# Kernel tuning notes

Measured on AMD Instinct MI355X. Metric: run time of the kernel, lower is better.

Reference implementation:

```python
import jax, jax.numpy as jnp
import numpy as np

N_NODES = 100000
N_EDGES = 1600000
IN_DIM = 128
HID = 128
NUM_LAYERS = 10
NUM_CLASSES = 2
NUM_GRAPHS = 64


def setup_inputs() -> dict:
    key = jax.random.key(0)
    ks = jax.random.split(key, 16)
    x = jax.random.normal(ks[0], (N_NODES, IN_DIM), dtype=jnp.float32)
    # edges with no self loops (GIN_Conv calls remove_self_loops)
    src = jax.random.randint(ks[1], (N_EDGES,), 0, N_NODES)
    off = jax.random.randint(ks[2], (N_EDGES,), 1, N_NODES)
    dst = (src + off) % N_NODES
    edge_index = jnp.stack([src, dst]).astype(jnp.int64)
    batch = jnp.sort(jax.random.randint(ks[3], (N_NODES,), 0, NUM_GRAPHS)).astype(jnp.int64)
    s = 1.0 / np.sqrt(HID)
    eps = jnp.zeros((NUM_LAYERS,), dtype=jnp.float32)
    W1 = jax.random.normal(ks[4], (NUM_LAYERS, IN_DIM, HID), dtype=jnp.float32) * s
    b1 = jnp.zeros((NUM_LAYERS, HID), dtype=jnp.float32)
    W2 = jax.random.normal(ks[5], (NUM_LAYERS, HID, HID), dtype=jnp.float32) * s
    b2 = jnp.zeros((NUM_LAYERS, HID), dtype=jnp.float32)
    Wc1 = jax.random.normal(ks[6], (HID, HID), dtype=jnp.float32) * s
    bc1 = jnp.zeros((HID,), dtype=jnp.float32)
    Wc2 = jax.random.normal(ks[7], (HID, NUM_CLASSES), dtype=jnp.float32) * s
    bc2 = jnp.zeros((NUM_CLASSES,), dtype=jnp.float32)
    return {"x": x, "edge_index": edge_index, "batch": batch, "eps": eps,
            "W1": W1, "b1": b1, "W2": W2, "b2": b2,
            "Wc1": Wc1, "bc1": bc1, "Wc2": Wc2, "bc2": bc2}


def _gin_block(x, src, dst, eps_i, W1_i, b1_i, W2_i, b2_i, mlp_residual):
    # gather-scatter add aggregation: aggr[v] = sum_{(u->v)} x[u]
    aggr = jax.ops.segment_sum(x[src], dst, num_segments=N_NODES)
    h = (1.0 + eps_i) * x + aggr
    out = jnp.dot(jax.nn.relu(jnp.dot(h, W1_i) + b1_i), W2_i) + b2_i
    if mlp_residual:  # MLP internal residual (layers i > 0)
        out = out + h
    out = jax.nn.relu(out)  # ResidualGNNBlock: Identity norm, relu, Identity dropout
    out = out + x  # block residual (dims match: in_dim == hidden)
    return out


def reference(x, edge_index, batch, eps, W1, b1, W2, b2, Wc1, bc1, Wc2, bc2):
    src, dst = edge_index[0], edge_index[1]
    for i in range(NUM_LAYERS):
        x = _gin_block(x, src, dst, eps[i], W1[i], b1[i], W2[i], b2[i], mlp_residual=(i > 0))
    # global_mean_pool
    sums = jax.ops.segment_sum(x, batch, num_segments=NUM_GRAPHS)
    cnts = jax.ops.segment_sum(jnp.ones((x.shape[0], 1), x.dtype), batch, num_segments=NUM_GRAPHS)
    pooled = sums / jnp.maximum(cnts, 1.0)
    # classifier MLP (dropout inactive in eval)
    logits = jnp.dot(jax.nn.relu(jnp.dot(pooled, Wc1) + bc1), Wc2) + bc2
    return logits
```

## Files before the change

### kernel.cpp

```cpp
#include <hip/hip_runtime.h>

#define N_NODES 100000
#define N_EDGES 1600000
#define HID 128
#define NUM_LAYERS 10
#define NUM_GRAPHS 64
#define SCAN_BLOCKS ((N_NODES + 255) / 256)


__global__ __launch_bounds__(256) void count_deg_kernel(const int* __restrict__ dst,
                                                        int* __restrict__ deg, int E) {
  int e = blockIdx.x * 256 + threadIdx.x;
  if (e < E) atomicAdd(&deg[dst[e]], 1);
}

__global__ __launch_bounds__(256) void block_sum_kernel(const int* __restrict__ deg,
                                                        int* __restrict__ psum, int n) {
  __shared__ int sd[256];
  int i = blockIdx.x * 256 + threadIdx.x;
  sd[threadIdx.x] = (i < n) ? deg[i] : 0;
  __syncthreads();
  for (int off = 128; off > 0; off >>= 1) {
    if (threadIdx.x < off) sd[threadIdx.x] += sd[threadIdx.x + off];
    __syncthreads();
  }
  if (threadIdx.x == 0) psum[blockIdx.x] = sd[0];
}

__global__ __launch_bounds__(512) void scan_partials_kernel(const int* __restrict__ psum,
                                                            int* __restrict__ poff, int nb) {
  __shared__ int sd[512];
  int i = threadIdx.x;
  int v = (i < nb) ? psum[i] : 0;
  sd[i] = v;
  __syncthreads();
  for (int off = 1; off < 512; off <<= 1) {
    int t = (i >= off) ? sd[i - off] : 0;
    __syncthreads();
    sd[i] += t;
    __syncthreads();
  }
  if (i < nb) poff[i] = sd[i] - v;
}

__global__ __launch_bounds__(256) void write_rs_kernel(const int* __restrict__ deg,
                                                       const int* __restrict__ poff,
                                                       int* __restrict__ rs, int n) {
  __shared__ int sd[256];
  int i = blockIdx.x * 256 + threadIdx.x;
  int v = (i < n) ? deg[i] : 0;
  sd[threadIdx.x] = v;
  __syncthreads();
  for (int off = 1; off < 256; off <<= 1) {
    int t = (threadIdx.x >= off) ? sd[threadIdx.x - off] : 0;
    __syncthreads();
    sd[threadIdx.x] += t;
    __syncthreads();
  }
  if (i < n) rs[i + 1] = poff[blockIdx.x] + sd[threadIdx.x];
  if (i == 0) rs[0] = 0;
}

__global__ __launch_bounds__(256) void copy_int_kernel(const int* __restrict__ a,
                                                       int* __restrict__ b, int n) {
  int i = blockIdx.x * 256 + threadIdx.x;
  if (i < n) b[i] = a[i];
}

__global__ __launch_bounds__(256) void fill_csr_kernel(const int* __restrict__ src,
                                                       const int* __restrict__ dst,
                                                       int* __restrict__ cur,
                                                       int* __restrict__ csr, int E) {
  int e = blockIdx.x * 256 + threadIdx.x;
  if (e < E) {
    int p = atomicAdd(&cur[dst[e]], 1);
    csr[p] = src[e];
  }
}


__global__ __launch_bounds__(256, 4) void layer_kernel(const float* __restrict__ xin,
                                                       float* __restrict__ xout,
                                                       const int* __restrict__ rs,
                                                       const int* __restrict__ csr,
                                                       const float* __restrict__ eps, int layer,
                                                       const float* __restrict__ W1,
                                                       const float* __restrict__ b1,
                                                       const float* __restrict__ W2,
                                                       const float* __restrict__ b2,
                                                       int n, int addH) {
  __shared__ float lh[64 * 128];
  const int tid = threadIdx.x;
  const int row0 = blockIdx.x * 64;
  const float4* x4 = (const float4*)xin;
  float4* lh4 = (float4*)lh;
  const float s = 1.0f + eps[layer];

  const int w = tid >> 5;
  const int lane = tid & 31;
#pragma unroll
  for (int it = 0; it < 8; ++it) {
    int li = it * 8 + w;
    int node = row0 + li;
    float ax = 0.f, ay = 0.f, az = 0.f, aw = 0.f;
    if (node < n) {
      float4 v = x4[node * 32 + lane];
      ax = v.x * s; ay = v.y * s; az = v.z * s; aw = v.w * s;
      int e = rs[node], e1 = rs[node + 1];
      for (; e + 1 < e1; e += 2) {
        int u0 = csr[e], u1 = csr[e + 1];
        float4 t0 = x4[u0 * 32 + lane];
        float4 t1 = x4[u1 * 32 + lane];
        ax += t0.x; ay += t0.y; az += t0.z; aw += t0.w;
        ax += t1.x; ay += t1.y; az += t1.z; aw += t1.w;
      }
      if (e < e1) {
        int u = csr[e];
        float4 t = x4[u * 32 + lane];
        ax += t.x; ay += t.y; az += t.z; aw += t.w;
      }
    }
    float4 r; r.x = ax; r.y = ay; r.z = az; r.w = aw;
    lh4[li * 32 + lane] = r;
  }
  __syncthreads();

  const int cg = tid & 31;
  const int rg = tid >> 5;
  float acc[8][4];
#pragma unroll
  for (int r = 0; r < 8; ++r) { acc[r][0] = acc[r][1] = acc[r][2] = acc[r][3] = 0.f; }

  for (int k4 = 0; k4 < 32; ++k4) {
    float4 w0 = *(const float4*)(W1 + (k4 * 4 + 0) * 128 + cg * 4);
    float4 w1 = *(const float4*)(W1 + (k4 * 4 + 1) * 128 + cg * 4);
    float4 w2 = *(const float4*)(W1 + (k4 * 4 + 2) * 128 + cg * 4);
    float4 w3 = *(const float4*)(W1 + (k4 * 4 + 3) * 128 + cg * 4);
#pragma unroll
    for (int r = 0; r < 8; ++r) {
      float4 a = *(const float4*)(lh + (rg * 8 + r) * 128 + k4 * 4);
      acc[r][0] += a.x * w0.x + a.y * w1.x + a.z * w2.x + a.w * w3.x;
      acc[r][1] += a.x * w0.y + a.y * w1.y + a.z * w2.y + a.w * w3.y;
      acc[r][2] += a.x * w0.z + a.y * w1.z + a.z * w2.z + a.w * w3.z;
      acc[r][3] += a.x * w0.w + a.y * w1.w + a.z * w2.w + a.w * w3.w;
    }
  }

  float4 hreg[8];
#pragma unroll
  for (int r = 0; r < 8; ++r) hreg[r] = *(const float4*)(lh + (rg * 8 + r) * 128 + cg * 4);
  __syncthreads();

  {
    float4 bb = *(const float4*)(b1 + cg * 4);
#pragma unroll
    for (int r = 0; r < 8; ++r) {
      float4 o;
      o.x = fmaxf(acc[r][0] + bb.x, 0.f);
      o.y = fmaxf(acc[r][1] + bb.y, 0.f);
      o.z = fmaxf(acc[r][2] + bb.z, 0.f);
      o.w = fmaxf(acc[r][3] + bb.w, 0.f);
      *(float4*)(lh + (rg * 8 + r) * 128 + cg * 4) = o;
      acc[r][0] = acc[r][1] = acc[r][2] = acc[r][3] = 0.f;
    }
  }
  __syncthreads();

  for (int k4 = 0; k4 < 32; ++k4) {
    float4 w0 = *(const float4*)(W2 + (k4 * 4 + 0) * 128 + cg * 4);
    float4 w1 = *(const float4*)(W2 + (k4 * 4 + 1) * 128 + cg * 4);
    float4 w2 = *(const float4*)(W2 + (k4 * 4 + 2) * 128 + cg * 4);
    float4 w3 = *(const float4*)(W2 + (k4 * 4 + 3) * 128 + cg * 4);
#pragma unroll
    for (int r = 0; r < 8; ++r) {
      float4 a = *(const float4*)(lh + (rg * 8 + r) * 128 + k4 * 4);
      acc[r][0] += a.x * w0.x + a.y * w1.x + a.z * w2.x + a.w * w3.x;
      acc[r][1] += a.x * w0.y + a.y * w1.y + a.z * w2.y + a.w * w3.y;
      acc[r][2] += a.x * w0.z + a.y * w1.z + a.z * w2.z + a.w * w3.z;
      acc[r][3] += a.x * w0.w + a.y * w1.w + a.z * w2.w + a.w * w3.w;
    }
  }

  float4 b2v = *(const float4*)(b2 + cg * 4);
  float4* xo4 = (float4*)xout;
#pragma unroll
  for (int r = 0; r < 8; ++r) {
    int row = row0 + rg * 8 + r;
    if (row < n) {
      float ox = acc[r][0] + b2v.x;
      float oy = acc[r][1] + b2v.y;
      float oz = acc[r][2] + b2v.z;
      float ow = acc[r][3] + b2v.w;
      if (addH) {
        ox += hreg[r].x; oy += hreg[r].y; oz += hreg[r].z; ow += hreg[r].w;
      }
      ox = fmaxf(ox, 0.f); oy = fmaxf(oy, 0.f); oz = fmaxf(oz, 0.f); ow = fmaxf(ow, 0.f);
      float4 xv = x4[row * 32 + cg];
      float4 o;
      o.x = ox + xv.x; o.y = oy + xv.y; o.z = oz + xv.z; o.w = ow + xv.w;
      xo4[row * 32 + cg] = o;
    }
  }
}


__global__ __launch_bounds__(128) void pool_kernel(const float* __restrict__ x,
                                                   const int* __restrict__ batch,
                                                   float* __restrict__ pool,
                                                   int* __restrict__ gcnt, int n) {
  const int CH = 512;
  int c = threadIdx.x;
  int n0 = blockIdx.x * CH;
  if (n0 >= n) return;
  int n1 = n0 + CH; if (n1 > n) n1 = n;
  float acc = 0.f;
  int g = batch[n0];
  int cl = 0;
  for (int i = n0; i < n1; ++i) {
    int gi = batch[i];
    if (gi != g) {
      atomicAdd(&pool[g * 128 + c], acc);
      if (c == 0) atomicAdd(&gcnt[g], cl);
      acc = 0.f; cl = 0; g = gi;
    }
    acc += x[i * 128 + c];
    cl++;
  }
  atomicAdd(&pool[g * 128 + c], acc);
  if (c == 0) atomicAdd(&gcnt[g], cl);
}


__global__ __launch_bounds__(128) void classifier_kernel(const float* __restrict__ pool,
                                                         const int* __restrict__ gcnt,
                                                         const float* __restrict__ Wc1,
                                                         const float* __restrict__ bc1,
                                                         const float* __restrict__ Wc2,
                                                         const float* __restrict__ bc2,
                                                         float* __restrict__ out) {
  __shared__ float prow[128];
  __shared__ float hid[128];
  int g = blockIdx.x;
  int c = threadIdx.x;
  float cf = (float)gcnt[g];
  if (cf < 1.f) cf = 1.f;
  prow[c] = pool[g * 128 + c] / cf;
  __syncthreads();
  float a = bc1[c];
  for (int k = 0; k < 128; ++k) a += prow[k] * Wc1[k * 128 + c];
  hid[c] = fmaxf(a, 0.f);
  __syncthreads();
  if (c < 2) {
    float a2 = bc2[c];
    for (int k = 0; k < 128; ++k) a2 += hid[k] * Wc2[k * 2 + c];
    out[g * 2 + c] = a2;
  }
}


extern "C" void kernel_launch(void* const* d_in, const int* in_sizes, int n_in,
                              void* d_out, int out_size, void* d_ws, size_t ws_size,
                              hipStream_t stream) {
  const float* x_in = (const float*)d_in[0];
  const int* edge_index = (const int*)d_in[1];
  const int* batch = (const int*)d_in[2];
  const float* eps = (const float*)d_in[3];
  const float* W1 = (const float*)d_in[4];
  const float* b1 = (const float*)d_in[5];
  const float* W2 = (const float*)d_in[6];
  const float* b2 = (const float*)d_in[7];
  const float* Wc1 = (const float*)d_in[8];
  const float* bc1 = (const float*)d_in[9];
  const float* Wc2 = (const float*)d_in[10];
  const float* bc2 = (const float*)d_in[11];
  float* out = (float*)d_out;

  const int N = N_NODES, E = N_EDGES;
  const int* src = edge_index;
  const int* dst = edge_index + E;

  float* xa = (float*)d_ws;
  float* xb = xa + (size_t)N * 128;
  int* deg = (int*)(xb + (size_t)N * 128);
  int* rs = deg + N;
  int* cur = rs + (N + 1);
  int* csr = cur + N;
  float* pool = (float*)(csr + E);
  int* gcnt = (int*)(pool + NUM_GRAPHS * 128);
  int* psum = gcnt + NUM_GRAPHS;
  int* poff = psum + SCAN_BLOCKS;

  hipMemcpyAsync(xa, x_in, (size_t)N * 128 * sizeof(float), hipMemcpyDeviceToDevice, stream);
  hipMemsetAsync(deg, 0, N * sizeof(int), stream);

  count_deg_kernel<<<(E + 255) / 256, 256, 0, stream>>>(dst, deg, E);
  block_sum_kernel<<<SCAN_BLOCKS, 256, 0, stream>>>(deg, psum, N);
  scan_partials_kernel<<<1, 512, 0, stream>>>(psum, poff, SCAN_BLOCKS);
  write_rs_kernel<<<SCAN_BLOCKS, 256, 0, stream>>>(deg, poff, rs, N);
  copy_int_kernel<<<(N + 255) / 256, 256, 0, stream>>>(rs, cur, N);
  fill_csr_kernel<<<(E + 255) / 256, 256, 0, stream>>>(src, dst, cur, csr, E);

  for (int i = 0; i < NUM_LAYERS; ++i) {
    const float* xi = (i % 2 == 0) ? xa : xb;
    float* xo = (i % 2 == 0) ? xb : xa;
    layer_kernel<<<(N + 63) / 64, 256, 0, stream>>>(xi, xo, rs, csr, eps, i,
                                                    W1 + (size_t)i * 128 * 128, b1 + (size_t)i * 128,
                                                    W2 + (size_t)i * 128 * 128, b2 + (size_t)i * 128,
                                                    N, i > 0 ? 1 : 0);
  }
  const float* xfin = (NUM_LAYERS % 2 == 0) ? xa : xb;

  hipMemsetAsync(pool, 0, NUM_GRAPHS * 128 * sizeof(float), stream);
  hipMemsetAsync(gcnt, 0, NUM_GRAPHS * sizeof(int), stream);
  pool_kernel<<<(N + 511) / 512, 128, 0, stream>>>(xfin, batch, pool, gcnt, N);
  classifier_kernel<<<NUM_GRAPHS, 128, 0, stream>>>(pool, gcnt, Wc1, bc1, Wc2, bc2, out);
}
```

Baseline: 2.786 ms.

## Unroll gather by four with index prefetch, fuse cursor init, drop input copy

The neighbor aggregation loop is unrolled to four gathers per iteration, and the next four CSR indices are loaded ahead so more row loads are in flight at once. The cursor array is written directly by the scan kernel, which removes the separate copy kernel. Layer 0 reads the input features directly instead of first copying 51 MB into the workspace, and the ping-pong buffers are adjusted to match. The occupancy hint is raised from 4 to 5 blocks per SM, which may force register spills in the fused MLP part.

New measurement: 2.811 ms. About the same (+0.9%).

```diff
diff --git a/kernel.cpp b/kernel.cpp
--- a/kernel.cpp
+++ b/kernel.cpp
@@ -45,7 +45,8 @@
 
 __global__ __launch_bounds__(256) void write_rs_kernel(const int* __restrict__ deg,
                                                        const int* __restrict__ poff,
-                                                       int* __restrict__ rs, int n) {
+                                                       int* __restrict__ rs,
+                                                       int* __restrict__ cur, int n) {
   __shared__ int sd[256];
   int i = blockIdx.x * 256 + threadIdx.x;
   int v = (i < n) ? deg[i] : 0;
@@ -57,14 +58,12 @@
     sd[threadIdx.x] += t;
     __syncthreads();
   }
-  if (i < n) rs[i + 1] = poff[blockIdx.x] + sd[threadIdx.x];
+  if (i < n) {
+    int incl = poff[blockIdx.x] + sd[threadIdx.x];
+    rs[i + 1] = incl;
+    cur[i] = incl - v;
+  }
   if (i == 0) rs[0] = 0;
-}
-
-__global__ __launch_bounds__(256) void copy_int_kernel(const int* __restrict__ a,
-                                                       int* __restrict__ b, int n) {
-  int i = blockIdx.x * 256 + threadIdx.x;
-  if (i < n) b[i] = a[i];
 }
 
 __global__ __launch_bounds__(256) void fill_csr_kernel(const int* __restrict__ src,
@@ -79,7 +78,7 @@
 }
 
 
-__global__ __launch_bounds__(256, 4) void layer_kernel(const float* __restrict__ xin,
+__global__ __launch_bounds__(256, 5) void layer_kernel(const float* __restrict__ xin,
                                                        float* __restrict__ xout,
                                                        const int* __restrict__ rs,
                                                        const int* __restrict__ csr,
@@ -106,16 +105,37 @@
     if (node < n) {
       float4 v = x4[node * 32 + lane];
       ax = v.x * s; ay = v.y * s; az = v.z * s; aw = v.w * s;
-      int e = rs[node], e1 = rs[node + 1];
-      for (; e + 1 < e1; e += 2) {
-        int u0 = csr[e], u1 = csr[e + 1];
-        float4 t0 = x4[u0 * 32 + lane];
-        float4 t1 = x4[u1 * 32 + lane];
-        ax += t0.x; ay += t0.y; az += t0.z; aw += t0.w;
-        ax += t1.x; ay += t1.y; az += t1.z; aw += t1.w;
+      const int e0 = rs[node];
+      const int m = rs[node + 1] - e0;
+      int i = 0;
+      if (m >= 4) {
+        int u0 = csr[e0], u1 = csr[e0 + 1], u2 = csr[e0 + 2], u3 = csr[e0 + 3];
+        for (; i + 8 <= m; i += 4) {
+          float4 t0 = x4[u0 * 32 + lane];
+          float4 t1 = x4[u1 * 32 + lane];
+          float4 t2 = x4[u2 * 32 + lane];
+          float4 t3 = x4[u3 * 32 + lane];
+          u0 = csr[e0 + i + 4]; u1 = csr[e0 + i + 5];
+          u2 = csr[e0 + i + 6]; u3 = csr[e0 + i + 7];
+          ax += t0.x + t1.x + t2.x + t3.x;
+          ay += t0.y + t1.y + t2.y + t3.y;
+          az += t0.z + t1.z + t2.z + t3.z;
+          aw += t0.w + t1.w + t2.w + t3.w;
+        }
+        {
+          float4 t0 = x4[u0 * 32 + lane];
+          float4 t1 = x4[u1 * 32 + lane];
+          float4 t2 = x4[u2 * 32 + lane];
+          float4 t3 = x4[u3 * 32 + lane];
+          ax += t0.x + t1.x + t2.x + t3.x;
+          ay += t0.y + t1.y + t2.y + t3.y;
+          az += t0.z + t1.z + t2.z + t3.z;
+          aw += t0.w + t1.w + t2.w + t3.w;
+          i += 4;
+        }
       }
-      if (e < e1) {
-        int u = csr[e];
+      for (; i < m; ++i) {
+        int u = csr[e0 + i];
         float4 t = x4[u * 32 + lane];
         ax += t.x; ay += t.y; az += t.z; aw += t.w;
       }
@@ -290,25 +310,23 @@
   int* psum = gcnt + NUM_GRAPHS;
   int* poff = psum + SCAN_BLOCKS;
 
-  hipMemcpyAsync(xa, x_in, (size_t)N * 128 * sizeof(float), hipMemcpyDeviceToDevice, stream);
   hipMemsetAsync(deg, 0, N * sizeof(int), stream);
 
   count_deg_kernel<<<(E + 255) / 256, 256, 0, stream>>>(dst, deg, E);
   block_sum_kernel<<<SCAN_BLOCKS, 256, 0, stream>>>(deg, psum, N);
   scan_partials_kernel<<<1, 512, 0, stream>>>(psum, poff, SCAN_BLOCKS);
-  write_rs_kernel<<<SCAN_BLOCKS, 256, 0, stream>>>(deg, poff, rs, N);
-  copy_int_kernel<<<(N + 255) / 256, 256, 0, stream>>>(rs, cur, N);
+  write_rs_kernel<<<SCAN_BLOCKS, 256, 0, stream>>>(deg, poff, rs, cur, N);
   fill_csr_kernel<<<(E + 255) / 256, 256, 0, stream>>>(src, dst, cur, csr, E);
 
   for (int i = 0; i < NUM_LAYERS; ++i) {
-    const float* xi = (i % 2 == 0) ? xa : xb;
-    float* xo = (i % 2 == 0) ? xb : xa;
+    const float* xi = (i == 0) ? x_in : ((i % 2 == 0) ? xb : xa);
+    float* xo = (i % 2 == 0) ? xa : xb;
     layer_kernel<<<(N + 63) / 64, 256, 0, stream>>>(xi, xo, rs, csr, eps, i,
                                                     W1 + (size_t)i * 128 * 128, b1 + (size_t)i * 128,
                                                     W2 + (size_t)i * 128 * 128, b2 + (size_t)i * 128,
                                                     N, i > 0 ? 1 : 0);
   }
-  const float* xfin = (NUM_LAYERS % 2 == 0) ? xa : xb;
+  const float* xfin = (NUM_LAYERS % 2 == 0) ? xb : xa;
 
   hipMemsetAsync(pool, 0, NUM_GRAPHS * 128 * sizeof(float), stream);
   hipMemsetAsync(gcnt, 0, NUM_GRAPHS * sizeof(int), stream);
```
